# Kernel tuning notes

Measured on AMD Instinct MI355X. Metric: run time of the kernel, lower is better.

## Reference

```python
import jax, jax.numpy as jnp
import numpy as np

POOL_RATIO = 0.25
ROUTING_NUM = 3
B, N, D, H = 32, 2048, 512, 512


def setup_inputs() -> dict:
    key = jax.random.key(0)
    k_x, k_adj, k_w = jax.random.split(key, 3)
    x = jax.random.normal(k_x, (B, N, D), dtype=jnp.float32)
    # variable node counts per graph; row 0 uses all N nodes so max_cluster is static
    rng = np.random.default_rng(0)
    lens = np.full(B, N, dtype=np.int64)
    lens[1:] = rng.integers(N // 2, N + 1, size=B - 1)
    mask_np = (np.arange(N)[None, :] < lens[:, None])  # [B,N] bool
    mask = jnp.asarray(mask_np)
    # sparse-ish random adjacency, zeroed outside the node mask
    adj = (jax.random.uniform(k_adj, (B, N, N)) < 0.01).astype(jnp.float32)
    m = mask.astype(jnp.float32)
    adj = adj * m[:, None, :] * m[:, :, None]
    W = jax.random.normal(k_w, (D, H), dtype=jnp.float32) * 0.02
    b = jnp.zeros((H,), dtype=jnp.float32)
    return {"x": x, "adj": adj, "W": W, "b": b, "mask": mask}


def masked_softmax(s, m):
    # m: bool broadcastable to s; masked entries -> exactly 0 probability
    s = jnp.where(m, s, jnp.float32(-1e9))
    return jax.nn.softmax(s, axis=-1) * m


def squash(s):
    # squash along last (feature) dim, as in torch sum(dim=2) on [B,C,H]
    mag_sq = jnp.sum(s * s, axis=-1, keepdims=True)
    mag = jnp.sqrt(mag_sq)
    return mag_sq / (1.0 + mag_sq) * (s / mag)


def reference(x, adj, W, b, mask):
    fmask = mask.astype(x.dtype)
    node_num = fmask.sum(axis=1)                               # [B]
    cluster_num = jnp.floor(node_num * POOL_RATIO).astype(jnp.int32)
    max_cluster = int(x.shape[1] * POOL_RATIO)                 # static (row 0 has N nodes)
    cmask = jnp.arange(max_cluster)[None, :] < cluster_num[:, None]  # [B,C] bool
    cm = cmask[:, None, :]                                     # [B,1,C]
    # embed: dense GCN layer  z = relu(adj @ x @ W + b)  -> [B,N,H]
    z = jax.nn.relu(jnp.einsum('bnm,bmd,dh->bnh', adj, x, W) + b)
    s = jax.random.normal(jax.random.key(42), (x.shape[0], x.shape[1], max_cluster), dtype=x.dtype)
    for _ in range(ROUTING_NUM):
        s = masked_softmax(s, cm)                              # [B,N,C]
        xnext = squash(jnp.einsum('bnc,bnh->bch', s, z))       # [B,C,H]
        s = s + jnp.einsum('bnh,bch->bnc', z, xnext)           # routing update
    return masked_softmax(s, cm)
```

## Files before the change

kernel.cpp:

```cpp
#include <hip/hip_runtime.h>
#include <cstdint>
#include <cstddef>

#define NB 32
#define NN 2048
#define ND 512
#define NH 512
#define NC 512
#define ROWS (NB*NN)

typedef __attribute__((ext_vector_type(8))) short short8v;
typedef __attribute__((ext_vector_type(4))) float f32x4;

#define MFMA16(a,b,c) __builtin_amdgcn_mfma_f32_16x16x32_bf16((a),(b),(c),0,0,0)

typedef const __attribute__((address_space(1))) unsigned int* gas_t;
typedef __attribute__((address_space(3))) unsigned int* las_t;

__device__ __forceinline__ void gload16(const void* g, void* l){
  __builtin_amdgcn_global_load_lds((gas_t)g, (las_t)l, 16, 0, 0);
}

__device__ __forceinline__ void fsplit(float v, unsigned short& h, unsigned short& l){
  unsigned u = __float_as_uint(v);
  unsigned hb = (u + 0x7FFFu + ((u>>16)&1u)) >> 16;
  float hf = __uint_as_float(hb<<16);
  float r = v - hf;
  unsigned ur = __float_as_uint(r);
  l = (unsigned short)((ur + 0x7FFFu + ((ur>>16)&1u)) >> 16);
  h = (unsigned short)hb;
}

__device__ __forceinline__ unsigned rotl32(unsigned x, int d){ return (x<<d)|(x>>(32-d)); }

__device__ __forceinline__ unsigned threefry_xor(unsigned k0, unsigned k1, unsigned c0, unsigned c1){
  unsigned ks2 = 0x1BD11BDAu ^ k0 ^ k1;
  unsigned x0 = c0 + k0, x1 = c1 + k1;
#define TF_RND(r) { x0 += x1; x1 = rotl32(x1,(r)); x1 ^= x0; }
  TF_RND(13) TF_RND(15) TF_RND(26) TF_RND(6)
  x0 += k1;  x1 += ks2 + 1u;
  TF_RND(17) TF_RND(29) TF_RND(16) TF_RND(24)
  x0 += ks2; x1 += k0 + 2u;
  TF_RND(13) TF_RND(15) TF_RND(26) TF_RND(6)
  x0 += k0;  x1 += k1 + 3u;
  TF_RND(17) TF_RND(29) TF_RND(16) TF_RND(24)
  x0 += k1;  x1 += ks2 + 4u;
  TF_RND(13) TF_RND(15) TF_RND(26) TF_RND(6)
  x0 += ks2; x1 += k0 + 5u;
#undef TF_RND
  return x0 ^ x1;
}

__device__ __forceinline__ float bits_to_normal(unsigned bits){
  float f = __uint_as_float((bits >> 9) | 0x3f800000u) - 1.0f;
  const float lo = -0.99999994f;
  float u = fmaxf(lo, fmaf(f, 2.0f, lo));
  float w = -log1pf(-(u*u));
  float p;
  if (w < 5.0f){
    w -= 2.5f;
    p =            2.81022636e-08f;
    p = fmaf(p, w, 3.43273939e-07f);
    p = fmaf(p, w, -3.5233877e-06f);
    p = fmaf(p, w, -4.39150654e-06f);
    p = fmaf(p, w, 0.00021858087f);
    p = fmaf(p, w, -0.00125372503f);
    p = fmaf(p, w, -0.00417768164f);
    p = fmaf(p, w, 0.246640727f);
    p = fmaf(p, w, 1.50140941f);
  } else {
    w = sqrtf(w) - 3.0f;
    p =            -0.000200214257f;
    p = fmaf(p, w, 0.000100950558f);
    p = fmaf(p, w, 0.00134934322f);
    p = fmaf(p, w, -0.00367342844f);
    p = fmaf(p, w, 0.00573950773f);
    p = fmaf(p, w, -0.0076224613f);
    p = fmaf(p, w, 0.00943887047f);
    p = fmaf(p, w, 1.00167406f);
    p = fmaf(p, w, 2.83297682f);
  }
  return 1.4142135623730951f * (p * u);
}

__global__ void __launch_bounds__(256) counts_kernel(const unsigned char* __restrict__ mraw,
                                                     int* __restrict__ cnum,
                                                     int* __restrict__ lenbuf){
  __shared__ int red[256];
  int b = blockIdx.x, tid = threadIdx.x;
  unsigned char b0 = mraw[0], b1 = mraw[1];
  int cnt = 0;
  if (b0 == 1 && b1 == 1){
    const unsigned char* p = mraw + (size_t)b * NN;
    for (int i = tid; i < NN; i += 256) cnt += (p[i] != 0);
  } else if (b0 == 1){
    const int* p = (const int*)mraw + (size_t)b * NN;
    for (int i = tid; i < NN; i += 256) cnt += (p[i] != 0);
  } else {
    const float* p = (const float*)mraw + (size_t)b * NN;
    for (int i = tid; i < NN; i += 256) cnt += (p[i] != 0.0f);
  }
  red[tid] = cnt; __syncthreads();
  for (int off = 128; off; off >>= 1){ if (tid < off) red[tid] += red[tid+off]; __syncthreads(); }
  if (tid == 0){ cnum[b] = red[0] >> 2; lenbuf[b] = red[0]; }
}

__global__ void __launch_bounds__(256) spmm_kernel(const float* __restrict__ adj,
                                                   const float* __restrict__ x,
                                                   unsigned short* __restrict__ yh,
                                                   unsigned short* __restrict__ yl,
                                                   const int* __restrict__ lenbuf){
  __shared__ int idxs[NN];
  __shared__ int wtot[4];
  int row = blockIdx.x;
  int b = row >> 11;
  int n = row & 2047;
  int tid = threadIdx.x;
  int l = tid & 63, w = tid >> 6;
  size_t base = (size_t)row * ND;
  if (n >= lenbuf[b]){
    yh[base+tid]=0; yl[base+tid]=0; yh[base+tid+256]=0; yl[base+tid+256]=0;
    return;
  }
  const float* arow = adj + (size_t)row * NN;
  float v[8];
  *(float4*)&v[0] = *(const float4*)(arow + tid*8);
  *(float4*)&v[4] = *(const float4*)(arow + tid*8 + 4);
  int lc = 0;
  #pragma unroll
  for (int j=0;j<8;j++) lc += (v[j] != 0.0f);
  int sc = lc;
  #pragma unroll
  for (int off=1; off<64; off<<=1){
    int t = __shfl_up(sc, off, 64);
    if (l >= off) sc += t;
  }
  if (l == 63) wtot[w] = sc;
  __syncthreads();
  int basep = 0;
  #pragma unroll
  for (int i=0;i<4;i++) if (i < w) basep += wtot[i];
  int total = wtot[0]+wtot[1]+wtot[2]+wtot[3];
  int pos = basep + sc - lc;
  #pragma unroll
  for (int j=0;j<8;j++){
    if (v[j] != 0.0f){ idxs[pos++] = tid*8 + j; }
  }
  __syncthreads();
  float acc0 = 0.f, acc1 = 0.f;
  const float* xb = x + (size_t)b * NN * ND;
  int j = 0;
  for (; j+4 <= total; j += 4){
    int m0_=idxs[j], m1_=idxs[j+1], m2_=idxs[j+2], m3_=idxs[j+3];
    float a0 = xb[(size_t)m0_*ND + tid], a1 = xb[(size_t)m1_*ND + tid];
    float a2 = xb[(size_t)m2_*ND + tid], a3 = xb[(size_t)m3_*ND + tid];
    float b0 = xb[(size_t)m0_*ND + tid + 256], b1 = xb[(size_t)m1_*ND + tid + 256];
    float b2 = xb[(size_t)m2_*ND + tid + 256], b3 = xb[(size_t)m3_*ND + tid + 256];
    acc0 += a0; acc0 += a1; acc0 += a2; acc0 += a3;
    acc1 += b0; acc1 += b1; acc1 += b2; acc1 += b3;
  }
  for (; j < total; j++){
    int m_ = idxs[j];
    acc0 += xb[(size_t)m_*ND + tid];
    acc1 += xb[(size_t)m_*ND + tid + 256];
  }
  unsigned short h,lo;
  fsplit(acc0,h,lo); yh[base+tid]=h;     yl[base+tid]=lo;
  fsplit(acc1,h,lo); yh[base+tid+256]=h; yl[base+tid+256]=lo;
}

__global__ void __launch_bounds__(256) wsplit_kernel(const float* __restrict__ W,
                                                     unsigned short* __restrict__ WTh,
                                                     unsigned short* __restrict__ WTl){
  __shared__ float t[32][33];
  int bx = blockIdx.x, by = blockIdx.y;
  int x = threadIdx.x & 31, y = threadIdx.x >> 5;
  for (int yy=y; yy<32; yy+=8) t[yy][x] = W[(size_t)(bx*32+yy)*512 + by*32 + x];
  __syncthreads();
  for (int yy=y; yy<32; yy+=8){
    float v = t[x][yy];
    unsigned short h,l; fsplit(v,h,l);
    size_t idx = (size_t)(by*32+yy)*512 + bx*32 + x;
    WTh[idx]=h; WTl[idx]=l;
  }
}

__global__ void __launch_bounds__(256) rngsm_kernel(unsigned short* __restrict__ sh,
                                                    unsigned short* __restrict__ sl,
                                                    const int* __restrict__ cnum){
  int row  = blockIdx.x*4 + (threadIdx.x >> 6);
  int lane = threadIdx.x & 63;
  int Kc = cnum[row >> 11];
  float e[8];
  #pragma unroll
  for (int j=0;j<8;j++){
    int c = (j<4) ? lane*4 + j : lane*4 + 252 + j;
    e[j] = bits_to_normal(threefry_xor(0u, 42u, 0u, (unsigned)row*512u + (unsigned)c));
  }
  float m = -3.0e38f;
  #pragma unroll
  for (int j=0;j<8;j++){
    int c = (j<4) ? lane*4 + j : lane*4 + 252 + j;
    if (c < Kc) m = fmaxf(m, e[j]);
  }
  #pragma unroll
  for (int off=32; off; off>>=1) m = fmaxf(m, __shfl_xor(m, off, 64));
  float r[8]; float sum = 0.f;
  #pragma unroll
  for (int j=0;j<8;j++){
    int c = (j<4) ? lane*4 + j : lane*4 + 252 + j;
    r[j] = (c < Kc) ? expf(e[j] - m) : 0.0f;
    sum += r[j];
  }
  #pragma unroll
  for (int off=32; off; off>>=1) sum += __shfl_xor(sum, off, 64);
  float inv = 1.0f / sum;
  #pragma unroll
  for (int j=0;j<8;j++) r[j] *= inv;
  unsigned long long ph=0, pl=0, qh=0, ql=0;
  #pragma unroll
  for (int j=0;j<4;j++){
    unsigned short h,l;
    fsplit(r[j],h,l);
    ph |= (unsigned long long)h << (16*j);  pl |= (unsigned long long)l << (16*j);
    fsplit(r[4+j],h,l);
    qh |= (unsigned long long)h << (16*j);  ql |= (unsigned long long)l << (16*j);
  }
  size_t base = (size_t)row * NC + lane*4;
  *(unsigned long long*)(sh + base)       = ph;
  *(unsigned long long*)(sl + base)       = pl;
  *(unsigned long long*)(sh + base + 256) = qh;
  *(unsigned long long*)(sl + base + 256) = ql;
}

template<bool SPLIT, bool WF32>
__global__ void __launch_bounds__(256) softmax_kernel(float* __restrict__ s,
                                                      unsigned short* __restrict__ sh,
                                                      unsigned short* __restrict__ sl,
                                                      const int* __restrict__ cnum){
  int row  = blockIdx.x*4 + (threadIdx.x >> 6);
  int lane = threadIdx.x & 63;
  int b = row >> 11;
  int Kc = cnum[b];
  float* p = s + (size_t)row * NC;
  float4 v0 = *(const float4*)(p + lane*4);
  float4 v1 = *(const float4*)(p + lane*4 + 256);
  float e[8] = {v0.x,v0.y,v0.z,v0.w,v1.x,v1.y,v1.z,v1.w};
  float m = -3.0e38f;
  #pragma unroll
  for (int j=0;j<8;j++){
    int c = (j<4) ? lane*4 + j : lane*4 + 252 + j;
    if (c < Kc) m = fmaxf(m, e[j]);
  }
  #pragma unroll
  for (int off=32; off; off>>=1) m = fmaxf(m, __shfl_xor(m, off, 64));
  float r[8]; float sum = 0.f;
  #pragma unroll
  for (int j=0;j<8;j++){
    int c = (j<4) ? lane*4 + j : lane*4 + 252 + j;
    r[j] = (c < Kc) ? expf(e[j] - m) : 0.0f;
    sum += r[j];
  }
  #pragma unroll
  for (int off=32; off; off>>=1) sum += __shfl_xor(sum, off, 64);
  float inv = 1.0f / sum;
  #pragma unroll
  for (int j=0;j<8;j++) r[j] *= inv;
  if constexpr (WF32){
    *(float4*)(p + lane*4)       = make_float4(r[0],r[1],r[2],r[3]);
    *(float4*)(p + lane*4 + 256) = make_float4(r[4],r[5],r[6],r[7]);
  }
  if constexpr (SPLIT){
    unsigned long long ph=0, pl=0, qh=0, ql=0;
    #pragma unroll
    for (int j=0;j<4;j++){
      unsigned short h,l;
      fsplit(r[j],h,l);
      ph |= (unsigned long long)h << (16*j);  pl |= (unsigned long long)l << (16*j);
      fsplit(r[4+j],h,l);
      qh |= (unsigned long long)h << (16*j);  ql |= (unsigned long long)l << (16*j);
    }
    size_t base = (size_t)row * NC + lane*4;
    *(unsigned long long*)(sh + base)       = ph;
    *(unsigned long long*)(sl + base)       = pl;
    *(unsigned long long*)(sh + base + 256) = qh;
    *(unsigned long long*)(sl + base + 256) = ql;
  }
}

template<int EPI>
__global__ void __launch_bounds__(256,2) gemmW_kernel(
    const unsigned short* __restrict__ Ah, const unsigned short* __restrict__ Al,
    const unsigned short* __restrict__ Bh, const unsigned short* __restrict__ Bl,
    unsigned short* __restrict__ OutH, unsigned short* __restrict__ OutL,
    float* __restrict__ Cf, const unsigned short* __restrict__ S2h,
    const unsigned short* __restrict__ S2l,
    const float* __restrict__ bias, const float* __restrict__ scale,
    const int* __restrict__ lenbuf, const int* __restrict__ cnumbuf,
    int K, long sA, long sB, long sC)
{
  __shared__ __align__(16) unsigned char smem[49152];
  int flat = blockIdx.x;
  int f2 = (flat & 7)*128 + (flat >> 3);
  int bx, by, bz;
  if constexpr (EPI==1){ bz = 0; bx = f2 >> 1; by = f2 & 1; }
  else { bz = f2 >> 5; int rem = f2 & 31; bx = rem >> 1; by = rem & 1; }
  Ah += (size_t)bz*sA; Al += (size_t)bz*sA;
  Bh += (size_t)bz*sB; Bl += (size_t)bz*sB;
  if constexpr (EPI==2){
    Cf += (size_t)bz*sC; S2h += (size_t)bz*sC; S2l += (size_t)bz*sC;
    scale += (size_t)bz*NC;
  }
  int m0 = bx*128, n0 = by*256;
  bool alive;
  if constexpr (EPI==1) alive = (m0 & 2047) < lenbuf[m0 >> 11];
  else                  alive = (m0 < lenbuf[bz]) && (n0 < cnumbuf[bz]);
  int tid = threadIdx.x;
  int l = tid & 63, wid = tid >> 6;
  int wr = wid >> 1, wc = wid & 1;
  int lr = l & 15, lk = l >> 4;

  f32x4 acc[4][8] = {};

  if (alive){
    int offA[4], offB[8];
    #pragma unroll
    for (int i=0;i<4;i++){
      int ra = wr*64 + i*16 + lr;
      offA[i] = ra*64 + ((lk ^ ((ra>>1)&3))<<4);
    }
    #pragma unroll
    for (int j=0;j<8;j++){
      int rb = wc*128 + j*16 + lr;
      offB[j] = rb*64 + ((lk ^ ((rb>>1)&3))<<4);
    }

    int srow = tid >> 2;
    int gslot = (tid & 3) ^ ((srow>>1)&3);
    const unsigned short* gAh = Ah + (size_t)(m0 + srow)*512 + gslot*8;
    const unsigned short* gAl = Al + (size_t)(m0 + srow)*512 + gslot*8;
    const unsigned short* gBh = Bh + (size_t)(n0 + srow)*512 + gslot*8;
    const unsigned short* gBl = Bl + (size_t)(n0 + srow)*512 + gslot*8;
    const size_t RS = (size_t)64*512;

#define STAGEW(k0) { \
    unsigned char* db = smem + wid*1024; \
    gload16(gAh + (k0),        db);           gload16(gAh + (k0) + RS,   db + 4096); \
    gload16(gAl + (k0),        db + 8192);    gload16(gAl + (k0) + RS,   db + 12288); \
    gload16(gBh + (k0),        db + 16384);   gload16(gBh + (k0) + RS,   db + 20480); \
    gload16(gBh + (k0) + 2*RS, db + 24576);   gload16(gBh + (k0) + 3*RS, db + 28672); \
    gload16(gBl + (k0),        db + 32768);   gload16(gBl + (k0) + RS,   db + 36864); \
    gload16(gBl + (k0) + 2*RS, db + 40960);   gload16(gBl + (k0) + 3*RS, db + 45056); }

    STAGEW(0)
    int KT = K >> 5;
    for (int t = 0; t < KT; ++t){
      asm volatile("s_waitcnt vmcnt(0)" ::: "memory");
      __syncthreads();
      short8v ah[4], al[4], bh[8], bl[8];
      #pragma unroll
      for (int i=0;i<4;i++){
        ah[i] = *(const short8v*)(smem + offA[i]);
        al[i] = *(const short8v*)(smem + 8192 + offA[i]);
      }
      #pragma unroll
      for (int j=0;j<8;j++){
        bh[j] = *(const short8v*)(smem + 16384 + offB[j]);
        bl[j] = *(const short8v*)(smem + 32768 + offB[j]);
      }
      __syncthreads();
      if (t+1 < KT) STAGEW((t+1)*32)
      __builtin_amdgcn_s_setprio(1);
      #pragma unroll
      for (int i=0;i<4;i++)
        #pragma unroll
        for (int j=0;j<8;j++) acc[i][j] = MFMA16(ah[i], bh[j], acc[i][j]);
      #pragma unroll
      for (int i=0;i<4;i++)
        #pragma unroll
        for (int j=0;j<8;j++) acc[i][j] = MFMA16(ah[i], bl[j], acc[i][j]);
      #pragma unroll
      for (int i=0;i<4;i++)
        #pragma unroll
        for (int j=0;j<8;j++) acc[i][j] = MFMA16(al[i], bh[j], acc[i][j]);
      __builtin_amdgcn_s_setprio(0);
    }
#undef STAGEW
  }

  float aux[8];
  #pragma unroll
  for (int j=0;j<8;j++){
    int gcol = n0 + wc*128 + j*16 + lr;
    if constexpr (EPI==1) aux[j] = bias[gcol];
    if constexpr (EPI==2) aux[j] = scale[gcol];
  }
  #pragma unroll
  for (int i=0;i<4;i++){
    #pragma unroll
    for (int r=0;r<4;r++){
      int grow = m0 + wr*64 + i*16 + lk*4 + r;
      size_t rowb = (size_t)grow*512 + n0 + wc*128 + lr;
      #pragma unroll
      for (int j=0;j<8;j++){
        float v = acc[i][j][r];
        if constexpr (EPI==1){
          v = fmaxf(v + aux[j], 0.f);
          unsigned short h,lo2; fsplit(v,h,lo2);
          OutH[rowb + j*16] = h; OutL[rowb + j*16] = lo2;
        } else {
          unsigned hh = S2h[rowb + j*16], ll = S2l[rowb + j*16];
          float s2 = __uint_as_float(hh<<16) + __uint_as_float(ll<<16);
          Cf[rowb + j*16] = s2 + aux[j]*v;
        }
      }
    }
  }
}

__global__ void __launch_bounds__(256,2) gemmT128_kernel(
    const unsigned short* __restrict__ Ah, const unsigned short* __restrict__ Al,
    const unsigned short* __restrict__ Bh, const unsigned short* __restrict__ Bl,
    unsigned short* __restrict__ OutH, unsigned short* __restrict__ OutL,
    float* __restrict__ parts, const int* __restrict__ lenbuf,
    const int* __restrict__ cnumbuf)
{
  __shared__ __align__(16) unsigned char smem[65536];
  int flat = blockIdx.x;
  int f2 = (flat & 7)*64 + (flat >> 3);
  int bz = f2 >> 4; int rem = f2 & 15; int bx = rem >> 2; int by = rem & 3;
  size_t boff = (size_t)bz * NN * 512;
  Ah += boff; Al += boff; Bh += boff; Bl += boff;
  int m0 = bx*128, n0 = by*128;
  int KT = (lenbuf[bz] + 31) >> 5;
  int limc = cnumbuf[bz] - m0;
  bool alive = (limc > 0);
  int tid = threadIdx.x;
  int l = tid & 63, wid = tid >> 6;
  int wr = wid >> 1, wc = wid & 1;
  int lr = l & 15, lk = l >> 4;

  f32x4 acc[4][4] = {};

  if (alive){
    bool liA[4];
    int offA[4], offB[4];
    #pragma unroll
    for (int i=0;i<4;i++){
      int ra = wr*64 + i*16 + lr;
      offA[i] = ra*64 + ((lk ^ ((ra>>1)&3) ^ ((ra>>3)&3))<<4);
      liA[i] = (wr*64 + i*16) < limc;
      int rb = wc*64 + i*16 + lr;
      offB[i] = rb*64 + ((lk ^ ((rb>>1)&3) ^ ((rb>>3)&3))<<4);
    }

    int np  = tid & 15;
    int seg = tid >> 4;

    short8v ra0h, ra1h, ra0l, ra1l, rb0h, rb1h, rb0l, rb1l;

#define TLOAD(k0) { \
    size_t ga = (size_t)((k0) + 2*np)*512 + m0 + seg*8; \
    ra0h = *(const short8v*)(Ah + ga); ra1h = *(const short8v*)(Ah + ga + 512); \
    ra0l = *(const short8v*)(Al + ga); ra1l = *(const short8v*)(Al + ga + 512); \
    size_t gb = (size_t)((k0) + 2*np)*512 + n0 + seg*8; \
    rb0h = *(const short8v*)(Bh + gb); rb1h = *(const short8v*)(Bh + gb + 512); \
    rb0l = *(const short8v*)(Bl + gb); rb1l = *(const short8v*)(Bl + gb + 512); }

#define TWRITE(buf) { \
    unsigned char* bb = smem + (buf)*32768; \
    _Pragma("unroll") \
    for (int k=0;k<8;k++){ \
      int c = seg*8 + k; \
      int ps = (np>>2) ^ ((c>>1)&3) ^ ((c>>3)&3); \
      int byo = c*64 + ps*16 + (np&3)*4; \
      *(unsigned int*)(bb + byo)         = (unsigned int)(unsigned short)ra0h[k] | ((unsigned int)(unsigned short)ra1h[k]<<16); \
      *(unsigned int*)(bb + 8192 + byo)  = (unsigned int)(unsigned short)ra0l[k] | ((unsigned int)(unsigned short)ra1l[k]<<16); \
      *(unsigned int*)(bb + 16384 + byo) = (unsigned int)(unsigned short)rb0h[k] | ((unsigned int)(unsigned short)rb1h[k]<<16); \
      *(unsigned int*)(bb + 24576 + byo) = (unsigned int)(unsigned short)rb0l[k] | ((unsigned int)(unsigned short)rb1l[k]<<16); } }

    TLOAD(0)
    TWRITE(0)
    __syncthreads();
    for (int t = 0; t < KT; ++t){
      int more = (t+1 < KT);
      if (more) TLOAD((t+1)*32)
      const unsigned char* base = smem + (t&1)*32768;
      short8v ah[4], bh[4], bl[4];
      #pragma unroll
      for (int i=0;i<4;i++) if (liA[i]) ah[i] = *(const short8v*)(base + offA[i]);
      #pragma unroll
      for (int j=0;j<4;j++){
        bh[j] = *(const short8v*)(base + 16384 + offB[j]);
        bl[j] = *(const short8v*)(base + 24576 + offB[j]);
      }
      __builtin_amdgcn_s_setprio(1);
      #pragma unroll
      for (int i=0;i<4;i++) if (liA[i])
        #pragma unroll
        for (int j=0;j<4;j++) acc[i][j] = MFMA16(ah[i], bh[j], acc[i][j]);
      #pragma unroll
      for (int i=0;i<4;i++) if (liA[i])
        #pragma unroll
        for (int j=0;j<4;j++) acc[i][j] = MFMA16(ah[i], bl[j], acc[i][j]);
      #pragma unroll
      for (int i=0;i<4;i++) if (liA[i]){
        short8v al = *(const short8v*)(base + 8192 + offA[i]);
        #pragma unroll
        for (int j=0;j<4;j++) acc[i][j] = MFMA16(al, bh[j], acc[i][j]);
      }
      __builtin_amdgcn_s_setprio(0);
      if (more) TWRITE((t+1)&1)
      __syncthreads();
    }
#undef TLOAD
#undef TWRITE
  }

  #pragma unroll
  for (int i=0;i<4;i++){
    #pragma unroll
    for (int r=0;r<4;r++){
      int grow = m0 + wr*64 + i*16 + lk*4 + r;
      float p = 0.f;
      size_t rowb = (size_t)bz*NC*NH + (size_t)grow*512 + n0 + wc*64 + lr;
      #pragma unroll
      for (int j=0;j<4;j++){
        float v = acc[i][j][r];
        p = fmaf(v,v,p);
        unsigned short h,lo2; fsplit(v,h,lo2);
        OutH[rowb + j*16] = h; OutL[rowb + j*16] = lo2;
      }
      p += __shfl_xor(p, 1, 64);
      p += __shfl_xor(p, 2, 64);
      p += __shfl_xor(p, 4, 64);
      p += __shfl_xor(p, 8, 64);
      if (lr == 0) parts[(((size_t)bz*NC) + grow)*8 + by*2 + wc] = p;
    }
  }
}

__global__ void __launch_bounds__(512) scale_kernel(const float* __restrict__ parts,
                                                    float* __restrict__ scale){
  int b = blockIdx.x, c = threadIdx.x;
  const float* p = parts + ((size_t)b*NC + c)*8;
  float m2 = ((p[0]+p[1])+(p[2]+p[3])) + ((p[4]+p[5])+(p[6]+p[7]));
  float sc = 0.0f;
  if (m2 > 0.0f) sc = (m2/(1.0f+m2)) / sqrtf(m2);
  scale[(size_t)b*NC + c] = sc;
}

extern "C" void kernel_launch(void* const* d_in, const int* in_sizes, int n_in,
                              void* d_out, int out_size, void* d_ws, size_t ws_size,
                              hipStream_t stream) {
  const float* x    = (const float*)d_in[0];
  const float* adj  = (const float*)d_in[1];
  const float* W    = (const float*)d_in[2];
  const float* bias = (const float*)d_in[3];
  const unsigned char* mask = (const unsigned char*)d_in[4];
  float* out = (float*)d_out;
  char* ws = (char*)d_ws;

  unsigned short* zh   = (unsigned short*)(ws);
  unsigned short* zl   = (unsigned short*)(ws + 67108864);
  unsigned short* sth  = (unsigned short*)(ws + 134217728);
  unsigned short* stl  = (unsigned short*)(ws + 201326592);
  unsigned short* xnh  = (unsigned short*)(ws + 268435456);
  unsigned short* xnl  = (unsigned short*)(ws + 285212672);
  unsigned short* WTh  = (unsigned short*)(ws + 301989888);
  unsigned short* WTl  = (unsigned short*)(ws + 302514176);
  float* parts         = (float*)(ws + 303038464);
  float* scalebuf      = (float*)(ws + 304087040);
  int*   cnum          = (int*)(ws + 304152576);
  int*   lenbuf        = (int*)(ws + 304152704);
  unsigned short* yh = sth;
  unsigned short* yl = stl;

  counts_kernel<<<NB, 256, 0, stream>>>(mask, cnum, lenbuf);
  wsplit_kernel<<<dim3(16,16), 256, 0, stream>>>(W, WTh, WTl);
  spmm_kernel<<<ROWS, 256, 0, stream>>>(adj, x, yh, yl, lenbuf);
  gemmW_kernel<1><<<1024, 256, 0, stream>>>(
      yh, yl, WTh, WTl, zh, zl, nullptr, nullptr, nullptr, bias, nullptr,
      lenbuf, cnum, ND, 0, 0, 0);

  for (int it = 0; it < 3; ++it){
    if (it == 0)
      rngsm_kernel<<<ROWS/4, 256, 0, stream>>>(sth, stl, cnum);
    else
      softmax_kernel<true,false><<<ROWS/4, 256, 0, stream>>>(out, sth, stl, cnum);
    gemmT128_kernel<<<512, 256, 0, stream>>>(
        sth, stl, zh, zl, xnh, xnl, parts, lenbuf, cnum);
    scale_kernel<<<NB, 512, 0, stream>>>(parts, scalebuf);
    gemmW_kernel<2><<<1024, 256, 0, stream>>>(
        zh, zl, xnh, xnl, nullptr, nullptr, out, sth, stl, nullptr, scalebuf,
        lenbuf, cnum, NH, (long)NN*NH, (long)NC*NH, (long)NN*NC);
  }
  softmax_kernel<false,true><<<ROWS/4, 256, 0, stream>>>(out, nullptr, nullptr, cnum);
}
```

Measured before the change: 1.293 ms.

## Double-buffer gemmW LDS tiles and split work over 8 waves

The gemmW kernel moves from 4 waves at two blocks per CU to 8 waves at one block per CU, so each wave computes a 64x64 sub-tile instead of 64x128. LDS grows to two 48KB buffers and the global-to-LDS loads are prefetched two k-steps ahead with partial vmcnt waits, so loads overlap the MFMA work. The goal is to hide memory latency in the GEMMs used for the embedding and the routing update. The cost is lower block-level occupancy, a larger LDS footprint, and more barriers per k-step.

Result: slower. 1.361 ms (+5.3%).

```diff
diff --git a/kernel.cpp b/kernel.cpp
--- a/kernel.cpp
+++ b/kernel.cpp
@@ -289,7 +289,7 @@
 }
 
 template<int EPI>
-__global__ void __launch_bounds__(256,2) gemmW_kernel(
+__global__ void __launch_bounds__(512,1) gemmW_kernel(
     const unsigned short* __restrict__ Ah, const unsigned short* __restrict__ Al,
     const unsigned short* __restrict__ Bh, const unsigned short* __restrict__ Bl,
     unsigned short* __restrict__ OutH, unsigned short* __restrict__ OutL,
@@ -299,7 +299,7 @@
     const int* __restrict__ lenbuf, const int* __restrict__ cnumbuf,
     int K, long sA, long sB, long sC)
 {
-  __shared__ __align__(16) unsigned char smem[49152];
+  __shared__ __align__(16) unsigned char smem[98304];
   int flat = blockIdx.x;
   int f2 = (flat & 7)*128 + (flat >> 3);
   int bx, by, bz;
@@ -317,22 +317,19 @@
   else                  alive = (m0 < lenbuf[bz]) && (n0 < cnumbuf[bz]);
   int tid = threadIdx.x;
   int l = tid & 63, wid = tid >> 6;
-  int wr = wid >> 1, wc = wid & 1;
+  int wr = wid >> 2, wc = wid & 3;
   int lr = l & 15, lk = l >> 4;
 
-  f32x4 acc[4][8] = {};
+  f32x4 acc[4][4] = {};
 
   if (alive){
-    int offA[4], offB[8];
+    int offA[4], offB[4];
     #pragma unroll
     for (int i=0;i<4;i++){
       int ra = wr*64 + i*16 + lr;
       offA[i] = ra*64 + ((lk ^ ((ra>>1)&3))<<4);
-    }
-    #pragma unroll
-    for (int j=0;j<8;j++){
-      int rb = wc*128 + j*16 + lr;
-      offB[j] = rb*64 + ((lk ^ ((rb>>1)&3))<<4);
+      int rb = wc*64 + i*16 + lr;
+      offB[i] = rb*64 + ((lk ^ ((rb>>1)&3))<<4);
     }
 
     int srow = tid >> 2;
@@ -341,57 +338,59 @@
     const unsigned short* gAl = Al + (size_t)(m0 + srow)*512 + gslot*8;
     const unsigned short* gBh = Bh + (size_t)(n0 + srow)*512 + gslot*8;
     const unsigned short* gBl = Bl + (size_t)(n0 + srow)*512 + gslot*8;
-    const size_t RS = (size_t)64*512;
-
-#define STAGEW(k0) { \
-    unsigned char* db = smem + wid*1024; \
-    gload16(gAh + (k0),        db);           gload16(gAh + (k0) + RS,   db + 4096); \
-    gload16(gAl + (k0),        db + 8192);    gload16(gAl + (k0) + RS,   db + 12288); \
-    gload16(gBh + (k0),        db + 16384);   gload16(gBh + (k0) + RS,   db + 20480); \
-    gload16(gBh + (k0) + 2*RS, db + 24576);   gload16(gBh + (k0) + 3*RS, db + 28672); \
-    gload16(gBl + (k0),        db + 32768);   gload16(gBl + (k0) + RS,   db + 36864); \
-    gload16(gBl + (k0) + 2*RS, db + 40960);   gload16(gBl + (k0) + 3*RS, db + 45056); }
-
-    STAGEW(0)
+    const size_t RS2 = (size_t)128*512;
+
+#define STAGEW(buf, k0) { \
+    unsigned char* db = smem + (buf)*49152 + wid*1024; \
+    gload16(gAh + (k0),       db); \
+    gload16(gAl + (k0),       db + 8192); \
+    gload16(gBh + (k0),       db + 16384); \
+    gload16(gBh + (k0) + RS2, db + 24576); \
+    gload16(gBl + (k0),       db + 32768); \
+    gload16(gBl + (k0) + RS2, db + 40960); }
+
     int KT = K >> 5;
+    STAGEW(0, 0)
+    if (KT > 1) STAGEW(1, 32)
     for (int t = 0; t < KT; ++t){
-      asm volatile("s_waitcnt vmcnt(0)" ::: "memory");
-      __syncthreads();
-      short8v ah[4], al[4], bh[8], bl[8];
+      if (t < KT-1) asm volatile("s_waitcnt vmcnt(6)" ::: "memory");
+      else          asm volatile("s_waitcnt vmcnt(0)" ::: "memory");
+      __builtin_amdgcn_s_barrier();
+      const unsigned char* base = smem + (t&1)*49152;
+      short8v ah[4], al[4], bh[4], bl[4];
       #pragma unroll
       for (int i=0;i<4;i++){
-        ah[i] = *(const short8v*)(smem + offA[i]);
-        al[i] = *(const short8v*)(smem + 8192 + offA[i]);
+        ah[i] = *(const short8v*)(base + offA[i]);
+        al[i] = *(const short8v*)(base + 8192 + offA[i]);
+        bh[i] = *(const short8v*)(base + 16384 + offB[i]);
+        bl[i] = *(const short8v*)(base + 32768 + offB[i]);
       }
-      #pragma unroll
-      for (int j=0;j<8;j++){
-        bh[j] = *(const short8v*)(smem + 16384 + offB[j]);
-        bl[j] = *(const short8v*)(smem + 32768 + offB[j]);
-      }
-      __syncthreads();
-      if (t+1 < KT) STAGEW((t+1)*32)
+      asm volatile("s_waitcnt lgkmcnt(0)" ::: "memory");
+      __builtin_amdgcn_sched_barrier(0);
+      __builtin_amdgcn_s_barrier();
+      if (t+2 < KT) STAGEW(t&1, (t+2)*32)
       __builtin_amdgcn_s_setprio(1);
       #pragma unroll
       for (int i=0;i<4;i++)
         #pragma unroll
-        for (int j=0;j<8;j++) acc[i][j] = MFMA16(ah[i], bh[j], acc[i][j]);
+        for (int j=0;j<4;j++) acc[i][j] = MFMA16(ah[i], bh[j], acc[i][j]);
       #pragma unroll
       for (int i=0;i<4;i++)
         #pragma unroll
-        for (int j=0;j<8;j++) acc[i][j] = MFMA16(ah[i], bl[j], acc[i][j]);
+        for (int j=0;j<4;j++) acc[i][j] = MFMA16(ah[i], bl[j], acc[i][j]);
       #pragma unroll
       for (int i=0;i<4;i++)
         #pragma unroll
-        for (int j=0;j<8;j++) acc[i][j] = MFMA16(al[i], bh[j], acc[i][j]);
+        for (int j=0;j<4;j++) acc[i][j] = MFMA16(al[i], bh[j], acc[i][j]);
       __builtin_amdgcn_s_setprio(0);
     }
 #undef STAGEW
   }
 
-  float aux[8];
-  #pragma unroll
-  for (int j=0;j<8;j++){
-    int gcol = n0 + wc*128 + j*16 + lr;
+  float aux[4];
+  #pragma unroll
+  for (int j=0;j<4;j++){
+    int gcol = n0 + wc*64 + j*16 + lr;
     if constexpr (EPI==1) aux[j] = bias[gcol];
     if constexpr (EPI==2) aux[j] = scale[gcol];
   }
@@ -400,9 +399,9 @@
     #pragma unroll
     for (int r=0;r<4;r++){
       int grow = m0 + wr*64 + i*16 + lk*4 + r;
-      size_t rowb = (size_t)grow*512 + n0 + wc*128 + lr;
-      #pragma unroll
-      for (int j=0;j<8;j++){
+      size_t rowb = (size_t)grow*512 + n0 + wc*64 + lr;
+      #pragma unroll
+      for (int j=0;j<4;j++){
         float v = acc[i][j][r];
         if constexpr (EPI==1){
           v = fmaxf(v + aux[j], 0.f);
@@ -579,7 +578,7 @@
   counts_kernel<<<NB, 256, 0, stream>>>(mask, cnum, lenbuf);
   wsplit_kernel<<<dim3(16,16), 256, 0, stream>>>(W, WTh, WTl);
   spmm_kernel<<<ROWS, 256, 0, stream>>>(adj, x, yh, yl, lenbuf);
-  gemmW_kernel<1><<<1024, 256, 0, stream>>>(
+  gemmW_kernel<1><<<1024, 512, 0, stream>>>(
       yh, yl, WTh, WTl, zh, zl, nullptr, nullptr, nullptr, bias, nullptr,
       lenbuf, cnum, ND, 0, 0, 0);
 
@@ -591,7 +590,7 @@
     gemmT128_kernel<<<512, 256, 0, stream>>>(
         sth, stl, zh, zl, xnh, xnl, parts, lenbuf, cnum);
     scale_kernel<<<NB, 512, 0, stream>>>(parts, scalebuf);
-    gemmW_kernel<2><<<1024, 256, 0, stream>>>(
+    gemmW_kernel<2><<<1024, 512, 0, stream>>>(
         zh, zl, xnh, xnl, nullptr, nullptr, out, sth, stl, nullptr, scalebuf,
         lenbuf, cnum, NH, (long)NN*NH, (long)NC*NH, (long)NN*NC);
   }
```
